# Optimization experiments

Hardware: AMD Instinct MI355X
Metric: run time of the kernel (lower is better)

The kernel has to match this reference:

```python
import jax, jax.numpy as jnp
import numpy as np

B, V, F, H = 8, 5023, 9976, 512  # batch, n_verts, n_faces, image size (K=1 face per pixel)


def _vertex_normals(verts, faces):
    # verts [V,3], faces [F,3] int. Faithful to DECA util.vertex_normals:
    # cross products scatter-added per face corner, then F.normalize(eps=1e-6).
    v0 = verts[faces[:, 0]]
    v1 = verts[faces[:, 1]]
    v2 = verts[faces[:, 2]]
    n = jnp.zeros_like(verts)
    n = n.at[faces[:, 1]].add(jnp.cross(v2 - v1, v0 - v1))
    n = n.at[faces[:, 2]].add(jnp.cross(v0 - v2, v1 - v2))
    n = n.at[faces[:, 0]].add(jnp.cross(v1 - v0, v2 - v0))
    norm = jnp.maximum(jnp.linalg.norm(n, axis=-1, keepdims=True), 1e-6)
    return n / norm


def _face_vertices(attr, faces):
    # attr [B,V,3] -> [B,F,3,3] gather of per-face corner attributes
    return jax.vmap(lambda a: a[faces])(attr)


def _rasterize_attributes(pix_to_face, bary, attributes):
    # attributes [B,F,3,D]; pix_to_face [N,H,W,K] packed face ids (-1 = miss);
    # bary [N,H,W,K,3]. Mirrors Pytorch3dRasterizer.forward post-raster math.
    Bn, Fn, _, D = attributes.shape
    attrs = attributes.reshape(Bn * Fn, 3, D)
    miss = pix_to_face < 0                              # [N,H,W,K]
    p2f = jnp.where(miss, 0, pix_to_face)
    pixel_face_vals = attrs[p2f]                        # [N,H,W,K,3,D] gather
    pixel_vals = jnp.sum(bary[..., None] * pixel_face_vals, axis=-2)  # [N,H,W,K,D]
    pixel_vals = jnp.where(miss[..., None], 0.0, pixel_vals)
    pixel_vals = jnp.moveaxis(pixel_vals[:, :, :, 0], -1, 1)          # [N,D,H,W]
    vismask = (pix_to_face[..., 0] > -1).astype(pixel_vals.dtype)[:, None]
    return jnp.concatenate([pixel_vals, vismask], axis=1)             # [N,D+1,H,W]


def setup_inputs() -> dict:
    keys = jax.random.split(jax.random.key(0), 8)
    vertices = jax.random.normal(keys[0], (B, V, 3), jnp.float32)
    transformed_vertices = jax.random.normal(keys[1], (B, V, 3), jnp.float32)
    albedos = jax.random.uniform(keys[2], (B, 3, 256, 256), jnp.float32)
    face_uvcoords = jax.random.uniform(keys[3], (F, 3, 3), jnp.float32) * 2.0 - 1.0
    bary = jax.random.uniform(keys[4], (B, H, H, 1, 3), jnp.float32) + 1e-3
    bary_coords = bary / bary.sum(-1, keepdims=True)
    faces = jax.random.randint(keys[5], (F, 3), 0, V, jnp.int32)
    p2f = jax.random.randint(keys[6], (B, H, H, 1), 0, B * F, jnp.int32)
    miss = jax.random.uniform(keys[7], (B, H, H, 1)) < 0.3
    pix_to_face = jnp.where(miss, jnp.int32(-1), p2f)
    return {"vertices": vertices, "transformed_vertices": transformed_vertices,
            "albedos": albedos, "face_uvcoords": face_uvcoords,
            "bary_coords": bary_coords, "faces": faces, "pix_to_face": pix_to_face}


def reference(vertices, transformed_vertices, albedos, face_uvcoords, bary_coords, faces, pix_to_face):
    # albedos is unused in this forward path (shading branch disabled in source).
    del albedos
    batch = vertices.shape[0]
    tv = transformed_vertices.at[:, :, 2].add(10.0)
    face_verts = _face_vertices(vertices, faces)                         # [B,F,3,3]
    normals = jax.vmap(_vertex_normals, in_axes=(0, None))(vertices, faces)
    face_normals = _face_vertices(normals, faces)                        # [B,F,3,3]
    t_normals = jax.vmap(_vertex_normals, in_axes=(0, None))(tv, faces)
    t_face_normals = _face_vertices(t_normals, faces)                    # [B,F,3,3]
    norm_uv = face_uvcoords * 0.5 + 0.5                                  # [F,3,3]
    attributes = jnp.concatenate([
        jnp.broadcast_to(norm_uv[None], (batch,) + norm_uv.shape),
        jax.lax.stop_gradient(t_face_normals),
        jax.lax.stop_gradient(face_verts),
        face_normals,
    ], axis=-1)                                                          # [B,F,3,12]
    rendering = _rasterize_attributes(pix_to_face, bary_coords, attributes)  # [B,13,H,W]
    uvcoords_images = rendering[:, :3]
    grid = jnp.transpose(uvcoords_images, (0, 2, 3, 1))[..., :2]
    t_normal_map = jax.lax.stop_gradient(rendering[:, 3:6])
    pos_mask = (t_normal_map[:, 2:] < -0.05).astype(rendering.dtype)
    normal_images = rendering[:, 9:12]
    return (uvcoords_images, pos_mask, grid, normals, normal_images, t_normals)
```

## Files before the change

kernel.cpp:

```cpp
#include <hip/hip_runtime.h>
#include <hip/hip_fp16.h>

#define BB_ 8
#define VV_ 5023
#define FF_ 9976
#define HH_ 512
#define K_ADJ 32

static constexpr long long OUT_UV   = 0;
static constexpr long long OUT_POS  = OUT_UV   + (long long)BB_*3*HH_*HH_;
static constexpr long long OUT_GRID = OUT_POS  + (long long)BB_*HH_*HH_;
static constexpr long long OUT_N    = OUT_GRID + (long long)BB_*HH_*HH_*2;
static constexpr long long OUT_NIMG = OUT_N    + (long long)BB_*VV_*3;
static constexpr long long OUT_TN   = OUT_NIMG + (long long)BB_*3*HH_*HH_;

typedef float __attribute__((ext_vector_type(4))) f4;
typedef int   __attribute__((ext_vector_type(4))) i4;

__device__ inline float pack_h2(float a, float b) {
    union { float f; __half2 h; } u;
    u.h = __halves2half2(__float2half_rn(a), __float2half_rn(b));
    return u.f;
}
__device__ inline float2 unpack_h2(float w) {
    union { float f; __half2 h; } u; u.f = w;
    return __half22float2(u.h);
}

__global__ __launch_bounds__(64) void facenorm3_k(const float* __restrict__ verts,
                                                  const float* __restrict__ tverts,
                                                  const int*   __restrict__ faces,
                                                  float4* __restrict__ fnorm,
                                                  int*    __restrict__ cnt,
                                                  int*    __restrict__ adj) {
    int t = blockIdx.x * 64 + threadIdx.x;
    if (t >= BB_ * 2 * FF_) return;
    int bm = t / FF_;
    int f  = t - bm * FF_;
    int m  = bm & 1;
    int b  = bm >> 1;

    int i0 = faces[f*3+0], i1 = faces[f*3+1], i2 = faces[f*3+2];

    const float* vb = (m ? tverts : verts) + (long long)b * VV_ * 3;
    const float zoff = m ? 10.0f : 0.0f;
    float v0x = vb[i0*3+0], v0y = vb[i0*3+1], v0z = vb[i0*3+2] + zoff;
    float v1x = vb[i1*3+0], v1y = vb[i1*3+1], v1z = vb[i1*3+2] + zoff;
    float v2x = vb[i2*3+0], v2y = vb[i2*3+1], v2z = vb[i2*3+2] + zoff;
    float ax = v1x - v0x, ay = v1y - v0y, az = v1z - v0z;
    float bx = v2x - v0x, by = v2y - v0y, bz = v2z - v0z;
    fnorm[(long long)t] = make_float4(ay*bz - az*by, az*bx - ax*bz, ax*by - ay*bx, 0.f);

    if (bm == 0) {
        int s0 = atomicAdd(&cnt[i0], 1); if (s0 < K_ADJ) adj[i0*K_ADJ + s0] = f;
        int s1 = atomicAdd(&cnt[i1], 1); if (s1 < K_ADJ) adj[i1*K_ADJ + s1] = f;
        int s2 = atomicAdd(&cnt[i2], 1); if (s2 < K_ADJ) adj[i2*K_ADJ + s2] = f;
    }
}

__global__ __launch_bounds__(64) void gather3_k(const int* __restrict__ cnt,
                                                const int* __restrict__ adj,
                                                const float4* __restrict__ fnorm,
                                                float* __restrict__ outN,
                                                float* __restrict__ outTN,
                                                float4* __restrict__ nbuf) {
    int t = blockIdx.x * 64 + threadIdx.x;
    if (t >= BB_ * 2 * VV_) return;
    int bm = t / VV_;
    int v  = t - bm * VV_;
    int m  = bm & 1;
    int b  = bm >> 1;

    int deg = min(cnt[v], K_ADJ);
    const float4* fb = fnorm + (long long)bm * FF_;
    float x = 0.f, y = 0.f, z = 0.f;
    for (int j = 0; j < deg; ++j) {
        int f = adj[v*K_ADJ + j];
        float4 a = fb[f];
        x += a.x; y += a.y; z += a.z;
    }
    float inv = 1.0f / fmaxf(sqrtf(x*x + y*y + z*z), 1e-6f);
    float nx = x * inv, ny = y * inv, nz = z * inv;

    long long idx = (long long)b * VV_ + v;
    float* nb = (float*)(nbuf + idx);
    if (m == 0) {
        float* o = outN + idx * 3;
        o[0] = nx; o[1] = ny; o[2] = nz;
        nb[0] = nx; nb[1] = ny; nb[2] = nz;
    } else {
        float* o = outTN + idx * 3;
        o[0] = nx; o[1] = ny; o[2] = nz;
        nb[3] = nz;
    }
}

__global__ __launch_bounds__(64) void build_rec64(const int*    __restrict__ faces,
                                                  const float*  __restrict__ uvc,
                                                  const float4* __restrict__ nbuf,
                                                  float4* __restrict__ rec) {
    int t = blockIdx.x * 64 + threadIdx.x;
    if (t >= BB_ * FF_) return;
    int b = t / FF_;
    int f = t - b * FF_;
    int ia = faces[f*3+0], ib = faces[f*3+1], ic = faces[f*3+2];

    const float4* nb = nbuf + (long long)b * VV_;
    float4 A = nb[ia], Bv = nb[ib], C = nb[ic];

    const float* u = uvc + (long long)f * 9;
    float r0 = u[0]*0.5f+0.5f, r1 = u[1]*0.5f+0.5f, r2 = u[2]*0.5f+0.5f;
    float r3 = u[3]*0.5f+0.5f, r4 = u[4]*0.5f+0.5f, r5 = u[5]*0.5f+0.5f;
    float r6 = u[6]*0.5f+0.5f, r7 = u[7]*0.5f+0.5f, r8 = u[8]*0.5f+0.5f;

    float4* o = rec + (long long)t * 4;
    o[0] = make_float4(A.w, Bv.w, C.w, pack_h2(r8, C.z));
    o[1] = make_float4(pack_h2(r0,r1), pack_h2(r2,r3), pack_h2(r4,r5), pack_h2(r6,r7));
    o[2] = make_float4(pack_h2(A.x,A.y), pack_h2(A.z,Bv.x), pack_h2(Bv.y,Bv.z), pack_h2(C.x,C.y));
}

__device__ __forceinline__ void shade(int pf, float w0, float w1, float w2,
                                      const float4* __restrict__ rec,
                                      float& uv0, float& uv1, float& uv2,
                                      float& n0, float& n1, float& n2, float& pm) {
    uv0 = uv1 = uv2 = n0 = n1 = n2 = pm = 0.0f;
    if (pf < 0) return;
    const float4* R = rec + (long long)pf * 4;
    float4 q0 = R[0], q1 = R[1], q2 = R[2];

    float2 u8c = unpack_h2(q0.w);
    float2 u01 = unpack_h2(q1.x), u23 = unpack_h2(q1.y);
    float2 u45 = unpack_h2(q1.z), u67 = unpack_h2(q1.w);
    float2 m01 = unpack_h2(q2.x), m23 = unpack_h2(q2.y);
    float2 m45 = unpack_h2(q2.z), m67 = unpack_h2(q2.w);

    uv0 = w0*u01.x + w1*u23.y + w2*u67.x;
    uv1 = w0*u01.y + w1*u45.x + w2*u67.y;
    uv2 = w0*u23.x + w1*u45.y + w2*u8c.x;
    n0  = w0*m01.x + w1*m23.y + w2*m67.x;
    n1  = w0*m01.y + w1*m45.x + w2*m67.y;
    n2  = w0*m23.x + w1*m45.y + w2*u8c.y;
    float tnz = w0*q0.x + w1*q0.y + w2*q0.z;
    pm = (tnz < -0.05f) ? 1.0f : 0.0f;
}

__global__ __launch_bounds__(256) void raster6(const i4* __restrict__ p2f4,
                                               const f4* __restrict__ bary4,
                                               const float4* __restrict__ rec,
                                               float* __restrict__ out) {
    int t = blockIdx.x * blockDim.x + threadIdx.x;
    const int NQ = BB_ * HH_ * HH_ / 4;
    if (t >= NQ) return;
    int pix0 = t << 2;
    int b    = pix0 >> 18;
    int yx0  = pix0 & (HH_*HH_ - 1);

    i4 pf = p2f4[t];
    f4 B0 = bary4[(long long)t*3 + 0];
    f4 B1 = bary4[(long long)t*3 + 1];
    f4 B2 = bary4[(long long)t*3 + 2];

    float uv0a, uv1a, uv2a, n0a, n1a, n2a, pma;
    float uv0b, uv1b, uv2b, n0b, n1b, n2b, pmb;
    float uv0c, uv1c, uv2c, n0c, n1c, n2c, pmc;
    float uv0d, uv1d, uv2d, n0d, n1d, n2d, pmd;

    shade(pf.x, B0.x, B0.y, B0.z, rec, uv0a, uv1a, uv2a, n0a, n1a, n2a, pma);
    shade(pf.y, B0.w, B1.x, B1.y, rec, uv0b, uv1b, uv2b, n0b, n1b, n2b, pmb);
    shade(pf.z, B1.z, B1.w, B2.x, rec, uv0c, uv1c, uv2c, n0c, n1c, n2c, pmc);
    shade(pf.w, B2.y, B2.z, B2.w, rec, uv0d, uv1d, uv2d, n0d, n1d, n2d, pmd);

    const long long HW = (long long)HH_ * HH_;
    f4 vuv0 = {uv0a, uv0b, uv0c, uv0d};
    f4 vuv1 = {uv1a, uv1b, uv1c, uv1d};
    f4 vuv2 = {uv2a, uv2b, uv2c, uv2d};
    f4 vpos = {pma,  pmb,  pmc,  pmd};
    f4 vg0  = {uv0a, uv1a, uv0b, uv1b};
    f4 vg1  = {uv0c, uv1c, uv0d, uv1d};
    f4 vn0  = {n0a, n0b, n0c, n0d};
    f4 vn1  = {n1a, n1b, n1c, n1d};
    f4 vn2  = {n2a, n2b, n2c, n2d};

    __builtin_nontemporal_store(vuv0, (f4*)(out + OUT_UV  + ((long long)(b*3+0))*HW + yx0));
    __builtin_nontemporal_store(vuv1, (f4*)(out + OUT_UV  + ((long long)(b*3+1))*HW + yx0));
    __builtin_nontemporal_store(vuv2, (f4*)(out + OUT_UV  + ((long long)(b*3+2))*HW + yx0));
    __builtin_nontemporal_store(vpos, (f4*)(out + OUT_POS + (long long)b*HW + yx0));
    float* gbase = out + OUT_GRID + ((long long)b*HW + yx0)*2;
    __builtin_nontemporal_store(vg0, (f4*)(gbase + 0));
    __builtin_nontemporal_store(vg1, (f4*)(gbase + 4));
    __builtin_nontemporal_store(vn0, (f4*)(out + OUT_NIMG + ((long long)(b*3+0))*HW + yx0));
    __builtin_nontemporal_store(vn1, (f4*)(out + OUT_NIMG + ((long long)(b*3+1))*HW + yx0));
    __builtin_nontemporal_store(vn2, (f4*)(out + OUT_NIMG + ((long long)(b*3+2))*HW + yx0));
}

extern "C" void kernel_launch(void* const* d_in, const int* in_sizes, int n_in,
                              void* d_out, int out_size, void* d_ws, size_t ws_size,
                              hipStream_t stream) {
    const float* vertices  = (const float*)d_in[0];
    const float* tvertices = (const float*)d_in[1];
    const float* face_uvc  = (const float*)d_in[3];
    const float* bary      = (const float*)d_in[4];
    const int*   faces     = (const int*)d_in[5];
    const int*   p2f       = (const int*)d_in[6];

    float* out = (float*)d_out;

    float4* rec   = (float4*)d_ws;
    float4* fnorm = rec + (size_t)BB_ * FF_ * 4;
    float4* nbuf  = fnorm + (size_t)BB_ * 2 * FF_;
    int*    cnt   = (int*)(nbuf + (size_t)BB_ * VV_);
    int*    adj   = cnt + VV_;

    hipMemsetAsync(cnt, 0, (size_t)VV_ * sizeof(int), stream);

    {
        int n = BB_ * 2 * FF_;
        facenorm3_k<<<(n + 63) / 64, 64, 0, stream>>>(vertices, tvertices, faces,
                                                      fnorm, cnt, adj);
    }
    {
        int n = BB_ * 2 * VV_;
        gather3_k<<<(n + 63) / 64, 64, 0, stream>>>(cnt, adj, fnorm,
                                                    out + OUT_N, out + OUT_TN, nbuf);
    }
    {
        int n = BB_ * FF_;
        build_rec64<<<(n + 63) / 64, 64, 0, stream>>>(faces, face_uvc, nbuf, rec);
    }
    {
        int nq = BB_ * HH_ * HH_ / 4;
        raster6<<<(nq + 255) / 256, 256, 0, stream>>>((const i4*)p2f, (const f4*)bary,
                                                      rec, out);
    }
}
```

Before: 63.42 us.

## Eliminate build_rec kernel by scattering vertex normals directly into face records

Removes the separate per-face record build kernel. The uv part of each record is now written in the face-normal kernel. The normal part is scattered from the vertex-gather kernel using corner-tagged adjacency entries, and the intermediate per-vertex normal buffer is dropped. This saves one launch and a gather pass, at the cost of scattered 2- and 4-byte writes to records and a per-thread adjacency array that may spill to scratch. It also relies on every face corner being present in the adjacency list (degree ≤ K_ADJ); overflowing vertices would leave record fields unwritten.

```diff
diff --git a/kernel.cpp b/kernel.cpp
--- a/kernel.cpp
+++ b/kernel.cpp
@@ -17,20 +17,30 @@
 typedef float __attribute__((ext_vector_type(4))) f4;
 typedef int   __attribute__((ext_vector_type(4))) i4;
 
+__device__ inline unsigned short h16(float x) {
+    __half h = __float2half_rn(x);
+    return *(unsigned short*)&h;
+}
+__device__ inline unsigned int pack2u(float a, float b) {
+    return (unsigned int)h16(a) | ((unsigned int)h16(b) << 16);
+}
 __device__ inline float pack_h2(float a, float b) {
-    union { float f; __half2 h; } u;
-    u.h = __halves2half2(__float2half_rn(a), __float2half_rn(b));
-    return u.f;
+    union { float f; unsigned int u; } w;
+    w.u = pack2u(a, b);
+    return w.f;
 }
 __device__ inline float2 unpack_h2(float w) {
     union { float f; __half2 h; } u; u.f = w;
     return __half22float2(u.h);
 }
 
-__global__ __launch_bounds__(64) void facenorm3_k(const float* __restrict__ verts,
+
+__global__ __launch_bounds__(64) void facenorm4_k(const float* __restrict__ verts,
                                                   const float* __restrict__ tverts,
                                                   const int*   __restrict__ faces,
+                                                  const float* __restrict__ uvc,
                                                   float4* __restrict__ fnorm,
+                                                  char*   __restrict__ rec,
                                                   int*    __restrict__ cnt,
                                                   int*    __restrict__ adj) {
     int t = blockIdx.x * 64 + threadIdx.x;
@@ -51,19 +61,30 @@
     float bx = v2x - v0x, by = v2y - v0y, bz = v2z - v0z;
     fnorm[(long long)t] = make_float4(ay*bz - az*by, az*bx - ax*bz, ax*by - ay*bx, 0.f);
 
+    if (m == 0) {
+        const float* u = uvc + (long long)f * 9;
+        float r0 = u[0]*0.5f+0.5f, r1 = u[1]*0.5f+0.5f, r2 = u[2]*0.5f+0.5f;
+        float r3 = u[3]*0.5f+0.5f, r4 = u[4]*0.5f+0.5f, r5 = u[5]*0.5f+0.5f;
+        float r6 = u[6]*0.5f+0.5f, r7 = u[7]*0.5f+0.5f, r8 = u[8]*0.5f+0.5f;
+        char* rb = rec + ((long long)b * FF_ + f) * 64;
+        *(float4*)(rb + 16) = make_float4(pack_h2(r0,r1), pack_h2(r2,r3),
+                                          pack_h2(r4,r5), pack_h2(r6,r7));
+        *(unsigned short*)(rb + 12) = h16(r8);
+    }
+
     if (bm == 0) {
-        int s0 = atomicAdd(&cnt[i0], 1); if (s0 < K_ADJ) adj[i0*K_ADJ + s0] = f;
-        int s1 = atomicAdd(&cnt[i1], 1); if (s1 < K_ADJ) adj[i1*K_ADJ + s1] = f;
-        int s2 = atomicAdd(&cnt[i2], 1); if (s2 < K_ADJ) adj[i2*K_ADJ + s2] = f;
-    }
-}
-
-__global__ __launch_bounds__(64) void gather3_k(const int* __restrict__ cnt,
+        int s0 = atomicAdd(&cnt[i0], 1); if (s0 < K_ADJ) adj[i0*K_ADJ + s0] = f*4 + 0;
+        int s1 = atomicAdd(&cnt[i1], 1); if (s1 < K_ADJ) adj[i1*K_ADJ + s1] = f*4 + 1;
+        int s2 = atomicAdd(&cnt[i2], 1); if (s2 < K_ADJ) adj[i2*K_ADJ + s2] = f*4 + 2;
+    }
+}
+
+__global__ __launch_bounds__(64) void gather4_k(const int* __restrict__ cnt,
                                                 const int* __restrict__ adj,
                                                 const float4* __restrict__ fnorm,
                                                 float* __restrict__ outN,
                                                 float* __restrict__ outTN,
-                                                float4* __restrict__ nbuf) {
+                                                char*  __restrict__ rec) {
     int t = blockIdx.x * 64 + threadIdx.x;
     if (t >= BB_ * 2 * VV_) return;
     int bm = t / VV_;
@@ -73,50 +94,49 @@
 
     int deg = min(cnt[v], K_ADJ);
     const float4* fb = fnorm + (long long)bm * FF_;
+    int e[K_ADJ];
     float x = 0.f, y = 0.f, z = 0.f;
     for (int j = 0; j < deg; ++j) {
-        int f = adj[v*K_ADJ + j];
-        float4 a = fb[f];
+        int ej = adj[v*K_ADJ + j];
+        e[j] = ej;
+        float4 a = fb[ej >> 2];
         x += a.x; y += a.y; z += a.z;
     }
     float inv = 1.0f / fmaxf(sqrtf(x*x + y*y + z*z), 1e-6f);
     float nx = x * inv, ny = y * inv, nz = z * inv;
 
     long long idx = (long long)b * VV_ + v;
-    float* nb = (float*)(nbuf + idx);
+    char* rbase = rec + (long long)b * FF_ * 64;
+
     if (m == 0) {
         float* o = outN + idx * 3;
         o[0] = nx; o[1] = ny; o[2] = nz;
-        nb[0] = nx; nb[1] = ny; nb[2] = nz;
+        unsigned int pxy = pack2u(nx, ny);
+        unsigned short hz = h16(nz);
+        unsigned short hx = h16(nx);
+        unsigned int pyz = pack2u(ny, nz);
+        for (int j = 0; j < deg; ++j) {
+            int f = e[j] >> 2, k = e[j] & 3;
+            char* rb = rbase + (long long)f * 64;
+            if (k == 0) {
+                *(unsigned int*)(rb + 32) = pxy;
+                *(unsigned short*)(rb + 36) = hz;
+            } else if (k == 1) {
+                *(unsigned short*)(rb + 38) = hx;
+                *(unsigned int*)(rb + 40) = pyz;
+            } else {
+                *(unsigned int*)(rb + 44) = pxy;
+                *(unsigned short*)(rb + 14) = hz;
+            }
+        }
     } else {
         float* o = outTN + idx * 3;
         o[0] = nx; o[1] = ny; o[2] = nz;
-        nb[3] = nz;
-    }
-}
-
-__global__ __launch_bounds__(64) void build_rec64(const int*    __restrict__ faces,
-                                                  const float*  __restrict__ uvc,
-                                                  const float4* __restrict__ nbuf,
-                                                  float4* __restrict__ rec) {
-    int t = blockIdx.x * 64 + threadIdx.x;
-    if (t >= BB_ * FF_) return;
-    int b = t / FF_;
-    int f = t - b * FF_;
-    int ia = faces[f*3+0], ib = faces[f*3+1], ic = faces[f*3+2];
-
-    const float4* nb = nbuf + (long long)b * VV_;
-    float4 A = nb[ia], Bv = nb[ib], C = nb[ic];
-
-    const float* u = uvc + (long long)f * 9;
-    float r0 = u[0]*0.5f+0.5f, r1 = u[1]*0.5f+0.5f, r2 = u[2]*0.5f+0.5f;
-    float r3 = u[3]*0.5f+0.5f, r4 = u[4]*0.5f+0.5f, r5 = u[5]*0.5f+0.5f;
-    float r6 = u[6]*0.5f+0.5f, r7 = u[7]*0.5f+0.5f, r8 = u[8]*0.5f+0.5f;
-
-    float4* o = rec + (long long)t * 4;
-    o[0] = make_float4(A.w, Bv.w, C.w, pack_h2(r8, C.z));
-    o[1] = make_float4(pack_h2(r0,r1), pack_h2(r2,r3), pack_h2(r4,r5), pack_h2(r6,r7));
-    o[2] = make_float4(pack_h2(A.x,A.y), pack_h2(A.z,Bv.x), pack_h2(Bv.y,Bv.z), pack_h2(C.x,C.y));
+        for (int j = 0; j < deg; ++j) {
+            int f = e[j] >> 2, k = e[j] & 3;
+            *(float*)(rbase + (long long)f * 64 + 4*k) = nz;
+        }
+    }
 }
 
 __device__ __forceinline__ void shade(int pf, float w0, float w1, float w2,
@@ -205,31 +225,26 @@
 
     float* out = (float*)d_out;
 
-    float4* rec   = (float4*)d_ws;
-    float4* fnorm = rec + (size_t)BB_ * FF_ * 4;
-    float4* nbuf  = fnorm + (size_t)BB_ * 2 * FF_;
-    int*    cnt   = (int*)(nbuf + (size_t)BB_ * VV_);
+    char*   rec   = (char*)d_ws;
+    float4* fnorm = (float4*)(rec + (size_t)BB_ * FF_ * 64);
+    int*    cnt   = (int*)(fnorm + (size_t)BB_ * 2 * FF_);
     int*    adj   = cnt + VV_;
 
     hipMemsetAsync(cnt, 0, (size_t)VV_ * sizeof(int), stream);
 
     {
         int n = BB_ * 2 * FF_;
-        facenorm3_k<<<(n + 63) / 64, 64, 0, stream>>>(vertices, tvertices, faces,
-                                                      fnorm, cnt, adj);
+        facenorm4_k<<<(n + 63) / 64, 64, 0, stream>>>(vertices, tvertices, faces,
+                                                      face_uvc, fnorm, rec, cnt, adj);
     }
     {
         int n = BB_ * 2 * VV_;
-        gather3_k<<<(n + 63) / 64, 64, 0, stream>>>(cnt, adj, fnorm,
-                                                    out + OUT_N, out + OUT_TN, nbuf);
-    }
-    {
-        int n = BB_ * FF_;
-        build_rec64<<<(n + 63) / 64, 64, 0, stream>>>(faces, face_uvc, nbuf, rec);
+        gather4_k<<<(n + 63) / 64, 64, 0, stream>>>(cnt, adj, fnorm,
+                                                    out + OUT_N, out + OUT_TN, rec);
     }
     {
         int nq = BB_ * HH_ * HH_ / 4;
         raster6<<<(nq + 255) / 256, 256, 0, stream>>>((const i4*)p2f, (const f4*)bary,
-                                                      rec, out);
-    }
-}
+                                                      (const float4*)rec, out);
+    }
+}
```

Result: slower. 68.49 us (+8.0%).
